# Performance work log

Hardware: AMD Instinct MI355X
Metric: run time of the kernel (lower is better)

## Reference

```python
import jax, jax.numpy as jnp
import numpy as np

N = 50000      # nodes per graph
E = 600000     # edges per graph
IN_DIM = 512
HID = 128
LAYERS = 2


def setup_inputs() -> dict:
    key = jax.random.key(0)
    ks = jax.random.split(key, 24)
    s = 0.05
    inp = {
        "src_fea": jax.random.normal(ks[0], (N, IN_DIM), jnp.float32),
        "trg_fea": jax.random.normal(ks[1], (N, IN_DIM), jnp.float32),
        "src_row": jax.random.randint(ks[2], (E,), 0, N, jnp.int32),
        "src_col": jax.random.randint(ks[3], (E,), 0, N, jnp.int32),
        "trg_row": jax.random.randint(ks[4], (E,), 0, N, jnp.int32),
        "trg_col": jax.random.randint(ks[5], (E,), 0, N, jnp.int32),
        # fx: Linear(in,hid)+GELU+Linear(hid,hid)+GELU
        "fxW1": jax.random.normal(ks[6], (IN_DIM, HID), jnp.float32) * s,
        "fxb1": jnp.zeros((HID,), jnp.float32),
        "fxW2": jax.random.normal(ks[7], (HID, HID), jnp.float32) * s,
        "fxb2": jnp.zeros((HID,), jnp.float32),
        # edge_att_mlp: Linear(2h,20)+ReLU+Linear(20,10)+ReLU+Linear(10,1)+ReLU
        "eaW1": jax.random.normal(ks[8], (2 * HID, 20), jnp.float32) * s,
        "eab1": jnp.zeros((20,), jnp.float32),
        "eaW2": jax.random.normal(ks[9], (20, 10), jnp.float32) * s,
        "eab2": jnp.zeros((10,), jnp.float32),
        "eaW3": jax.random.normal(ks[10], (10, 1), jnp.float32) * s,
        "eab3": jnp.zeros((1,), jnp.float32),
        # GraphConv (PyG-style, bias=False): out = x@Wroot + agg@Wrel
        "convWroot": jax.random.normal(ks[11], (LAYERS, HID, HID), jnp.float32) * s,
        "convWrel": jax.random.normal(ks[12], (LAYERS, HID, HID), jnp.float32) * s,
    }
    return inp


def _fx(x, W1, b1, W2, b2):
    h = jax.nn.gelu(x @ W1 + b1, approximate=False)
    return jax.nn.gelu(h @ W2 + b2, approximate=False)


def _edge_att(e, eaW1, eab1, eaW2, eab2, eaW3, eab3):
    h = jax.nn.relu(e @ eaW1 + eab1)
    h = jax.nn.relu(h @ eaW2 + eab2)
    h = jax.nn.relu(h @ eaW3 + eab3)
    return jax.nn.sigmoid(h)  # [E,1]


def _graph_conv(x, row, col, ew, Wroot, Wrel):
    # message from source (row) gathered, weighted, aggregated at target (col)
    msg = ew[:, None] * x[row]                                  # [E,h]
    agg = jax.ops.segment_sum(msg, col, num_segments=N)         # [N,h]
    return x @ Wroot + agg @ Wrel


def _branch(x0, row, col, convWroot, convWrel, eaW1, eab1, eaW2, eab2, eaW3, eab3, hard):
    xs, cfds = [], []
    x = x0
    for i in range(LAYERS):
        edge_rep = jnp.concatenate([x[row], x[col]], axis=-1)    # [E,2h]
        att = _edge_att(edge_rep, eaW1, eab1, eaW2, eab2, eaW3, eab3)[:, 0]
        wc = (att + hard) * 0.5
        wo = 1.0 - wc
        x = jax.nn.soft_sign(_graph_conv(x, row, col, wc, convWroot[i], convWrel[i]))
        cfd = jax.nn.soft_sign(_graph_conv(x, row, col, wo, convWroot[i], convWrel[i]))
        xs.append(x)
        cfds.append(cfd)
    return xs, cfds


def reference(src_fea, trg_fea, src_row, src_col, trg_row, trg_col,
              fxW1, fxb1, fxW2, fxb2,
              eaW1, eab1, eaW2, eab2, eaW3, eab3,
              convWroot, convWrel):
    src1 = _fx(src_fea, fxW1, fxb1, fxW2, fxb2)
    trg1 = _fx(trg_fea, fxW1, fxb1, fxW2, fxb2)
    ea = (eaW1, eab1, eaW2, eab2, eaW3, eab3)
    xs_s, cf_s = _branch(src1, src_row, src_col, convWroot, convWrel, *ea, 0.0)
    xs_t, cf_t = _branch(trg1, trg_row, trg_col, convWroot, convWrel, *ea, 0.0)
    # stack: [src1, xs_s..., trg1, xs_t..., cf_s..., cf_t...] -> [2+2*LAYERS+2*LAYERS? no: 10, N, h]
    return jnp.stack([src1] + xs_s + [trg1] + xs_t + cf_s + cf_t, axis=0)
```

## Files before the change

kernel.cpp:

```cpp
#include <hip/hip_runtime.h>
#include <math.h>
#include <stdint.h>


typedef __attribute__((ext_vector_type(8))) short bh8;
typedef __attribute__((ext_vector_type(4))) float f4;

__device__ __forceinline__ float relu_f(float x) { return x > 0.f ? x : 0.f; }

__device__ __forceinline__ unsigned short f2bf(float f) {
    union { float f; unsigned u; } v; v.f = f;
    unsigned r = v.u + 0x7FFF + ((v.u >> 16) & 1);
    return (unsigned short)(r >> 16);
}
__device__ __forceinline__ float bf2f(unsigned short b) {
    union { unsigned u; float f; } v; v.u = ((unsigned)b) << 16;
    return v.f;
}

template<int ACT>
__device__ __forceinline__ float act_fn(float x) {
    if (ACT == 1) return 0.5f * x * (1.f + erff(x * 0.70710678118654752f));
    if (ACT == 2) return x / (1.f + fabsf(x));
    return x;
}

__device__ __forceinline__ void emit_p_phase(short* As, short* Bs,
                                             const short* __restrict__ W56,
                                             short* __restrict__ P,
                                             int row0, int M, int t)
{
    #pragma unroll
    for (int p = 0; p < 4; ++p) {
        int idx = t + 256 * p;
        int r = idx >> 4;
        int c = (idx & 15) * 8;
        *(bh8*)&Bs[r * 136 + c] = *(const bh8*)(W56 + r * 128 + c);
    }
    __syncthreads();
    const int lane = t & 63, w = t >> 6, l15 = lane & 15, l4 = lane >> 4;
    f4 accP[4];
    #pragma unroll
    for (int ni = 0; ni < 4; ++ni) accP[ni] = (f4){0.f, 0.f, 0.f, 0.f};
    #pragma unroll
    for (int kk = 0; kk < 4; ++kk) {
        bh8 a = *(const bh8*)&As[(w * 16 + l15) * 136 + kk * 32 + l4 * 8];
        #pragma unroll
        for (int ni = 0; ni < 4; ++ni) {
            bh8 b = *(const bh8*)&Bs[(ni * 16 + l15) * 136 + kk * 32 + l4 * 8];
            accP[ni] = __builtin_amdgcn_mfma_f32_16x16x32_bf16(a, b, accP[ni], 0, 0, 0);
        }
    }
    #pragma unroll
    for (int ni = 0; ni < 4; ++ni) {
        int col = ni * 16 + l15;
        #pragma unroll
        for (int r = 0; r < 4; ++r) {
            int row = row0 + w * 16 + l4 * 4 + r;
            if (row < M) P[(size_t)row * 64 + col] = (short)f2bf(accP[ni][r]);
        }
    }
}

template<int K, int AF, int ACT, bool BIAS, bool WF32, bool WB16, bool EMITP>
__global__ __launch_bounds__(256, 2)
void mfma_gemm(const void* __restrict__ X0a, const void* __restrict__ X0b,
               const short* __restrict__ W0t, const float* __restrict__ bias,
               float* __restrict__ outfA, short* __restrict__ outbA,
               float* __restrict__ outfB, short* __restrict__ outbB,
               const short* __restrict__ W56,
               short* __restrict__ PA, short* __restrict__ PB, int M)
{
    constexpr int BK  = 64;
    constexpr int LDA = EMITP ? 136 : 72;
    __shared__ short As[64 * LDA];
    __shared__ short Bs[128 * 72];

    const int half = gridDim.x >> 1;
    int bid = blockIdx.x;
    const int g1 = bid >= half;
    bid -= g1 ? half : 0;
    const void* X0v = g1 ? X0b : X0a;
    float* outf = g1 ? outfB : outfA;
    short* outb = g1 ? outbB : outbA;
    short* P    = g1 ? PB : PA;

    const int t    = threadIdx.x;
    const int row0 = bid * 64;
    const int lane = t & 63;
    const int w    = t >> 6;
    const int wr   = w & 1;
    const int wc   = w >> 1;
    const int l15  = lane & 15;
    const int l4   = lane >> 4;

    f4 acc[2][4];
    #pragma unroll
    for (int i = 0; i < 2; ++i)
        #pragma unroll
        for (int j = 0; j < 4; ++j)
            acc[i][j] = (f4){0.f, 0.f, 0.f, 0.f};

    const int ar = t >> 3;
    const int ac = (t & 7) * 8;

    #pragma unroll 1
    for (int k0 = 0; k0 < K; k0 += BK) {
        __syncthreads();
        #pragma unroll
        for (int p = 0; p < 2; ++p) {
            int r    = ar + p * 32;
            int grow = row0 + r;
            bh8 sv = {0, 0, 0, 0, 0, 0, 0, 0};
            if (AF == 0) {
                if (grow < M) {
                    const float* src = (const float*)X0v + (size_t)grow * K + k0 + ac;
                    float4 v0 = *(const float4*)src;
                    float4 v1 = *(const float4*)(src + 4);
                    sv[0] = (short)f2bf(v0.x); sv[1] = (short)f2bf(v0.y);
                    sv[2] = (short)f2bf(v0.z); sv[3] = (short)f2bf(v0.w);
                    sv[4] = (short)f2bf(v1.x); sv[5] = (short)f2bf(v1.y);
                    sv[6] = (short)f2bf(v1.z); sv[7] = (short)f2bf(v1.w);
                }
            } else {
                if (grow < M)
                    sv = *(const bh8*)((const short*)X0v + (size_t)grow * K + k0 + ac);
            }
            *(bh8*)&As[r * LDA + ac] = sv;
        }
        #pragma unroll
        for (int p = 0; p < 4; ++p) {
            int r = ar + p * 32;
            *(bh8*)&Bs[r * 72 + ac] = *(const bh8*)(W0t + (size_t)r * K + k0 + ac);
        }
        __syncthreads();
        #pragma unroll
        for (int kk = 0; kk < 2; ++kk) {
            bh8 a[2], b[4];
            #pragma unroll
            for (int mi = 0; mi < 2; ++mi)
                a[mi] = *(const bh8*)&As[(wr*32 + mi*16 + l15) * LDA + kk*32 + l4*8];
            #pragma unroll
            for (int ni = 0; ni < 4; ++ni)
                b[ni] = *(const bh8*)&Bs[(wc*64 + ni*16 + l15) * 72 + kk*32 + l4*8];
            #pragma unroll
            for (int mi = 0; mi < 2; ++mi)
                #pragma unroll
                for (int ni = 0; ni < 4; ++ni)
                    acc[mi][ni] = __builtin_amdgcn_mfma_f32_16x16x32_bf16(
                        a[mi], b[ni], acc[mi][ni], 0, 0, 0);
        }
    }

    if (EMITP) __syncthreads();
    #pragma unroll
    for (int mi = 0; mi < 2; ++mi) {
        #pragma unroll
        for (int ni = 0; ni < 4; ++ni) {
            int col = wc * 64 + ni * 16 + l15;
            float bv = BIAS ? bias[col] : 0.f;
            #pragma unroll
            for (int r = 0; r < 4; ++r) {
                int rloc = wr * 32 + mi * 16 + l4 * 4 + r;
                int row  = row0 + rloc;
                float v = act_fn<ACT>(acc[mi][ni][r] + bv);
                unsigned short bb = f2bf(v);
                if (row < M) {
                    if (WF32) outf[(size_t)row * 128 + col] = v;
                    if (WB16) outb[(size_t)row * 128 + col] = (short)bb;
                }
                if (EMITP) As[rloc * LDA + col] = (short)bb;
            }
        }
    }
    if (EMITP) emit_p_phase(As, Bs, W56, P, row0, M, t);
}

template<int MODE, bool WB16, bool EMITP>
__global__ __launch_bounds__(256, 2)
void conv_fused(const short* __restrict__ XbA, const short* __restrict__ XbB,
                const int* __restrict__ coffA, const int* __restrict__ coffB,
                const int* __restrict__ crowA, const int* __restrict__ crowB,
                const float* __restrict__ attcA, const float* __restrict__ attcB,
                const short* __restrict__ Wroot, const short* __restrict__ Wrel,
                const short* __restrict__ W56,
                float* __restrict__ outfA, float* __restrict__ outfB,
                short* __restrict__ outbA, short* __restrict__ outbB,
                short* __restrict__ PA, short* __restrict__ PB, int M)
{
    constexpr int LDA = 136;
    __shared__ short As[64 * LDA];
    __shared__ short Bs[128 * 72];

    const int half = gridDim.x >> 1;
    int bid = blockIdx.x;
    const int g1 = bid >= half;
    bid -= g1 ? half : 0;
    const short* Xb   = g1 ? XbB   : XbA;
    const int*   coff = g1 ? coffB : coffA;
    const int*   crow = g1 ? crowB : crowA;
    const float* attc = g1 ? attcB : attcA;
    float* outf = g1 ? outfB : outfA;
    short* outb = g1 ? outbB : outbA;
    short* P    = g1 ? PB : PA;

    const int t    = threadIdx.x;
    const int row0 = bid * 64;
    const int lane = t & 63;
    const int w    = t >> 6;
    const int wr   = w & 1;
    const int wc   = w >> 1;
    const int l15  = lane & 15;
    const int l4   = lane >> 4;

    {
        const int g  = t >> 4;
        const int li = t & 15;
        #pragma unroll 1
        for (int q = 0; q < 4; ++q) {
            int rloc = g * 4 + q;
            int n = row0 + rloc;
            float a8[8] = {0.f, 0.f, 0.f, 0.f, 0.f, 0.f, 0.f, 0.f};
            if (n < M) {
                int p  = coff[n];
                int pe = coff[n + 1];
                for (; p + 3 < pe; p += 4) {
                    float w0 = attc[p],     w1 = attc[p + 1];
                    float w2 = attc[p + 2], w3 = attc[p + 3];
                    int r0 = crow[p],     r1 = crow[p + 1];
                    int r2 = crow[p + 2], r3 = crow[p + 3];
                    w0 = MODE ? fmaf(-0.5f, w0, 1.f) : 0.5f * w0;
                    w1 = MODE ? fmaf(-0.5f, w1, 1.f) : 0.5f * w1;
                    w2 = MODE ? fmaf(-0.5f, w2, 1.f) : 0.5f * w2;
                    w3 = MODE ? fmaf(-0.5f, w3, 1.f) : 0.5f * w3;
                    bh8 v0 = *(const bh8*)&Xb[(size_t)r0 * 128 + li * 8];
                    bh8 v1 = *(const bh8*)&Xb[(size_t)r1 * 128 + li * 8];
                    bh8 v2 = *(const bh8*)&Xb[(size_t)r2 * 128 + li * 8];
                    bh8 v3 = *(const bh8*)&Xb[(size_t)r3 * 128 + li * 8];
                    #pragma unroll
                    for (int j = 0; j < 8; ++j) {
                        a8[j] = fmaf(w0, bf2f((unsigned short)v0[j]), a8[j]);
                        a8[j] = fmaf(w1, bf2f((unsigned short)v1[j]), a8[j]);
                        a8[j] = fmaf(w2, bf2f((unsigned short)v2[j]), a8[j]);
                        a8[j] = fmaf(w3, bf2f((unsigned short)v3[j]), a8[j]);
                    }
                }
                for (; p < pe; ++p) {
                    float w0 = attc[p];
                    int   r0 = crow[p];
                    w0 = MODE ? fmaf(-0.5f, w0, 1.f) : 0.5f * w0;
                    bh8 v0 = *(const bh8*)&Xb[(size_t)r0 * 128 + li * 8];
                    #pragma unroll
                    for (int j = 0; j < 8; ++j)
                        a8[j] = fmaf(w0, bf2f((unsigned short)v0[j]), a8[j]);
                }
            }
            bh8 o;
            #pragma unroll
            for (int j = 0; j < 8; ++j) o[j] = (short)f2bf(a8[j]);
            *(bh8*)&As[rloc * LDA + li * 8] = o;
        }
    }
    __syncthreads();

    f4 acc[2][4];
    #pragma unroll
    for (int i = 0; i < 2; ++i)
        #pragma unroll
        for (int j = 0; j < 4; ++j)
            acc[i][j] = (f4){0.f, 0.f, 0.f, 0.f};

    const int ar = t >> 3;
    const int ac = (t & 7) * 8;

    #pragma unroll 1
    for (int k0 = 0; k0 < 128; k0 += 64) {
        if (k0) __syncthreads();
        #pragma unroll
        for (int p = 0; p < 4; ++p) {
            int r = ar + p * 32;
            *(bh8*)&Bs[r * 72 + ac] = *(const bh8*)(Wrel + (size_t)r * 128 + k0 + ac);
        }
        __syncthreads();
        #pragma unroll
        for (int kk = 0; kk < 2; ++kk) {
            bh8 a[2], b[4];
            #pragma unroll
            for (int mi = 0; mi < 2; ++mi)
                a[mi] = *(const bh8*)&As[(wr*32 + mi*16 + l15) * LDA + k0 + kk*32 + l4*8];
            #pragma unroll
            for (int ni = 0; ni < 4; ++ni)
                b[ni] = *(const bh8*)&Bs[(wc*64 + ni*16 + l15) * 72 + kk*32 + l4*8];
            #pragma unroll
            for (int mi = 0; mi < 2; ++mi)
                #pragma unroll
                for (int ni = 0; ni < 4; ++ni)
                    acc[mi][ni] = __builtin_amdgcn_mfma_f32_16x16x32_bf16(
                        a[mi], b[ni], acc[mi][ni], 0, 0, 0);
        }
    }

    #pragma unroll 1
    for (int k0 = 0; k0 < 128; k0 += 64) {
        __syncthreads();
        #pragma unroll
        for (int p = 0; p < 2; ++p) {
            int r    = ar + p * 32;
            int grow = row0 + r;
            bh8 sv = {0, 0, 0, 0, 0, 0, 0, 0};
            if (grow < M)
                sv = *(const bh8*)(Xb + (size_t)grow * 128 + k0 + ac);
            *(bh8*)&As[r * LDA + ac] = sv;
        }
        #pragma unroll
        for (int p = 0; p < 4; ++p) {
            int r = ar + p * 32;
            *(bh8*)&Bs[r * 72 + ac] = *(const bh8*)(Wroot + (size_t)r * 128 + k0 + ac);
        }
        __syncthreads();
        #pragma unroll
        for (int kk = 0; kk < 2; ++kk) {
            bh8 a[2], b[4];
            #pragma unroll
            for (int mi = 0; mi < 2; ++mi)
                a[mi] = *(const bh8*)&As[(wr*32 + mi*16 + l15) * LDA + kk*32 + l4*8];
            #pragma unroll
            for (int ni = 0; ni < 4; ++ni)
                b[ni] = *(const bh8*)&Bs[(wc*64 + ni*16 + l15) * 72 + kk*32 + l4*8];
            #pragma unroll
            for (int mi = 0; mi < 2; ++mi)
                #pragma unroll
                for (int ni = 0; ni < 4; ++ni)
                    acc[mi][ni] = __builtin_amdgcn_mfma_f32_16x16x32_bf16(
                        a[mi], b[ni], acc[mi][ni], 0, 0, 0);
        }
    }

    if (EMITP) __syncthreads();
    #pragma unroll
    for (int mi = 0; mi < 2; ++mi) {
        #pragma unroll
        for (int ni = 0; ni < 4; ++ni) {
            int col = wc * 64 + ni * 16 + l15;
            #pragma unroll
            for (int r = 0; r < 4; ++r) {
                int rloc = wr * 32 + mi * 16 + l4 * 4 + r;
                int row  = row0 + rloc;
                float v = act_fn<2>(acc[mi][ni][r]);
                unsigned short bb = f2bf(v);
                if (row < M) {
                    outf[(size_t)row * 128 + col] = v;
                    if (WB16) outb[(size_t)row * 128 + col] = (short)bb;
                }
                if (EMITP) As[rloc * LDA + col] = (short)bb;
            }
        }
    }
    if (EMITP) emit_p_phase(As, Bs, W56, P, row0, M, t);
}

__global__ void prep_all(const float* __restrict__ eaW1, const float* __restrict__ fxW1,
                         const float* __restrict__ fxW2, const float* __restrict__ convWroot,
                         const float* __restrict__ convWrel,
                         short* __restrict__ w56, short* __restrict__ fxW1t,
                         short* __restrict__ fxW2t, short* __restrict__ wrt,
                         short* __restrict__ wlt)
{
    int i = blockIdx.x * 256 + threadIdx.x;
    if (i < 64 * 128) {
        int j = i >> 7, k = i & 127;
        float v = 0.f;
        if (j < 20)                  v = eaW1[k * 20 + j];
        else if (j >= 32 && j < 52)  v = eaW1[(128 + k) * 20 + (j - 32)];
        w56[i] = (short)f2bf(v);
        return;
    }
    i -= 64 * 128;
    if (i < 512 * 128) {
        int k = i >> 7, n = i & 127;
        fxW1t[(size_t)n * 512 + k] = (short)f2bf(fxW1[i]);
        return;
    }
    i -= 512 * 128;
    if (i < 128 * 128) {
        int k = i >> 7, n = i & 127;
        fxW2t[n * 128 + k] = (short)f2bf(fxW2[i]);
        return;
    }
    i -= 128 * 128;
    if (i < 2 * 128 * 128) {
        int L = i >> 14, r = i & 16383;
        int k = r >> 7, n = r & 127;
        wrt[L * 16384 + n * 128 + k] = (short)f2bf(convWroot[i]);
        return;
    }
    i -= 2 * 128 * 128;
    if (i < 2 * 128 * 128) {
        int L = i >> 14, r = i & 16383;
        int k = r >> 7, n = r & 127;
        wlt[L * 16384 + n * 128 + k] = (short)f2bf(convWrel[i]);
    }
}

__global__ __launch_bounds__(256)
void edge_att_both(const short* __restrict__ PS, const short* __restrict__ PT,
                   const int* __restrict__ rowS, const int* __restrict__ colS,
                   const int* __restrict__ rowT, const int* __restrict__ colT,
                   const int* __restrict__ eposS, const int* __restrict__ eposT,
                   const float* __restrict__ eab1, const float* __restrict__ eaW2,
                   const float* __restrict__ eab2, const float* __restrict__ eaW3,
                   const float* __restrict__ eab3,
                   float* __restrict__ attcS, float* __restrict__ attcT, int E)
{
    __shared__ float w2[200], b2s[10], w3s[10], sb1[20], sb3;
    int t = threadIdx.x;
    if (t < 200) w2[t] = eaW2[t];
    if (t < 20)  sb1[t] = eab1[t];
    if (t < 10)  { b2s[t] = eab2[t]; w3s[t] = eaW3[t]; }
    if (t == 0)  sb3 = eab3[0];
    __syncthreads();

    int idx = blockIdx.x * 256 + t;
    if (idx >= 2 * E) return;
    const int g1 = idx >= E;
    const int e  = idx - (g1 ? E : 0);
    const short* P    = g1 ? PT : PS;
    const int*   row  = g1 ? rowT : rowS;
    const int*   col  = g1 ? colT : colS;
    const int*   epos = g1 ? eposT : eposS;
    float*       attc = g1 ? attcT : attcS;

    int r = row[e], c = col[e];
    const unsigned short* p1 = (const unsigned short*)P + (size_t)r * 64;
    const unsigned short* p2 = (const unsigned short*)P + (size_t)c * 64 + 32;

    bh8 a0 = *(const bh8*)&p1[0];
    bh8 a1 = *(const bh8*)&p1[8];
    ushort4 a2 = *(const ushort4*)&p1[16];
    bh8 b0 = *(const bh8*)&p2[0];
    bh8 b1 = *(const bh8*)&p2[8];
    ushort4 b2 = *(const ushort4*)&p2[16];

    float h1[20];
    #pragma unroll
    for (int j = 0; j < 8; ++j)
        h1[j] = relu_f(bf2f((unsigned short)a0[j]) + bf2f((unsigned short)b0[j]) + sb1[j]);
    #pragma unroll
    for (int j = 0; j < 8; ++j)
        h1[8 + j] = relu_f(bf2f((unsigned short)a1[j]) + bf2f((unsigned short)b1[j]) + sb1[8 + j]);
    h1[16] = relu_f(bf2f(a2.x) + bf2f(b2.x) + sb1[16]);
    h1[17] = relu_f(bf2f(a2.y) + bf2f(b2.y) + sb1[17]);
    h1[18] = relu_f(bf2f(a2.z) + bf2f(b2.z) + sb1[18]);
    h1[19] = relu_f(bf2f(a2.w) + bf2f(b2.w) + sb1[19]);

    float h3 = sb3;
    #pragma unroll
    for (int j2 = 0; j2 < 10; ++j2) {
        float s = b2s[j2];
        #pragma unroll
        for (int j = 0; j < 20; ++j)
            s = fmaf(h1[j], w2[j * 10 + j2], s);
        h3 = fmaf(relu_f(s), w3s[j2], h3);
    }
    h3 = relu_f(h3);
    attc[epos[e]] = 1.f / (1.f + expf(-h3));
}

__global__ void hist_both(const int* __restrict__ colS, const int* __restrict__ colT,
                          int* __restrict__ deg, int N, int E)
{
    int idx = blockIdx.x * 256 + threadIdx.x;
    if (idx >= 2 * E) return;
    const int g1 = idx >= E;
    const int e  = idx - (g1 ? E : 0);
    int c = (g1 ? colT : colS)[e];
    atomicAdd(&deg[(size_t)g1 * N + c], 1);
}

__device__ __forceinline__ int block_incl_scan(int v, int* wsum)
{
    int lane = threadIdx.x & 63;
    int w    = threadIdx.x >> 6;
    #pragma unroll
    for (int off = 1; off < 64; off <<= 1) {
        int t = __shfl_up(v, off);
        if (lane >= off) v += t;
    }
    if (lane == 63) wsum[w] = v;
    __syncthreads();
    int add = 0;
    for (int j = 0; j < w; ++j) add += wsum[j];
    return v + add;
}

__global__ __launch_bounds__(256)
void scanA_both(const int* __restrict__ deg, int* __restrict__ coffS,
                int* __restrict__ coffT, int* __restrict__ bsum, int N)
{
    __shared__ int wsum[4];
    int gy = blockIdx.y;
    const int* d = deg + (size_t)gy * N;
    int* coff    = gy ? coffT : coffS;
    int* bs      = bsum + gy * 256;
    int i = blockIdx.x * 256 + threadIdx.x;
    int orig = (i < N) ? d[i] : 0;
    int v = block_incl_scan(orig, wsum);
    if (i < N) coff[i] = v - orig;
    if (threadIdx.x == 255) bs[blockIdx.x] = v;
}

__global__ __launch_bounds__(256)
void scanB_both(const int* __restrict__ bsum, int* __restrict__ boff, int nb)
{
    __shared__ int wsum[4];
    int gy = blockIdx.y;
    const int* bs = bsum + gy * 256;
    int* bo       = boff + gy * 256;
    int tid = threadIdx.x;
    int orig = (tid < nb) ? bs[tid] : 0;
    int v = block_incl_scan(orig, wsum);
    if (tid < nb) bo[tid] = v - orig;
}

__global__ __launch_bounds__(256)
void scanC_both(int* __restrict__ coffS, int* __restrict__ coffT,
                const int* __restrict__ boff, int* __restrict__ curS,
                int* __restrict__ curT, int N, int E)
{
    int gy = blockIdx.y;
    int* coff = gy ? coffT : coffS;
    int* cur  = gy ? curT  : curS;
    const int* bo = boff + gy * 256;
    int i = blockIdx.x * 256 + threadIdx.x;
    if (i < N) {
        int v = coff[i] + bo[i >> 8];
        coff[i] = v;
        cur[i]  = v;
    }
    if (i == 0) coff[N] = E;
}

__global__ __launch_bounds__(256)
void fill_both(const int* __restrict__ rowS, const int* __restrict__ colS,
               const int* __restrict__ rowT, const int* __restrict__ colT,
               int* __restrict__ curS, int* __restrict__ curT,
               int* __restrict__ crowS, int* __restrict__ crowT,
               int* __restrict__ eposS, int* __restrict__ eposT, int E)
{
    int idx = blockIdx.x * 256 + threadIdx.x;
    if (idx >= 2 * E) return;
    const int g1 = idx >= E;
    const int e  = idx - (g1 ? E : 0);
    const int* row = g1 ? rowT : rowS;
    const int* col = g1 ? colT : colS;
    int* cur  = g1 ? curT  : curS;
    int* crow = g1 ? crowT : crowS;
    int* epos = g1 ? eposT : eposS;
    int c = col[e];
    int p = atomicAdd(&cur[c], 1);
    crow[p] = row[e];
    epos[e] = p;
}


extern "C" void kernel_launch(void* const* d_in, const int* in_sizes, int n_in,
                              void* d_out, int out_size, void* d_ws, size_t ws_size,
                              hipStream_t stream)
{
    const float* src_fea = (const float*)d_in[0];
    const float* trg_fea = (const float*)d_in[1];
    const int*   src_row = (const int*)d_in[2];
    const int*   src_col = (const int*)d_in[3];
    const int*   trg_row = (const int*)d_in[4];
    const int*   trg_col = (const int*)d_in[5];
    const float* fxW1 = (const float*)d_in[6];
    const float* fxb1 = (const float*)d_in[7];
    const float* fxW2 = (const float*)d_in[8];
    const float* fxb2 = (const float*)d_in[9];
    const float* eaW1 = (const float*)d_in[10];
    const float* eab1 = (const float*)d_in[11];
    const float* eaW2 = (const float*)d_in[12];
    const float* eab2 = (const float*)d_in[13];
    const float* eaW3 = (const float*)d_in[14];
    const float* eab3 = (const float*)d_in[15];
    const float* convWroot = (const float*)d_in[16];
    const float* convWrel  = (const float*)d_in[17];

    const int N = in_sizes[0] / 512;
    const int E = in_sizes[2];

    float* out = (float*)d_out;
    const size_t slot_sz = (size_t)N * 128;
    auto slot = [&](int i) { return out + (size_t)i * slot_sz; };

    float* fp    = (float*)d_ws;
    float* attcS = fp; fp += E;
    float* attcT = fp; fp += E;
    int* ip    = (int*)fp;
    int* deg   = ip; ip += 2 * N;
    int* bsum  = ip; ip += 512;
    int* boff  = ip; ip += 512;
    int* coffS = ip; ip += N + 2;
    int* coffT = ip; ip += N + 2;
    int* curS  = ip; ip += N;
    int* curT  = ip; ip += N;
    int* crowS = ip; ip += E;
    int* crowT = ip; ip += E;
    int* eposS = ip; ip += E;
    int* eposT = ip; ip += E;
    short* sp = (short*)((((uintptr_t)ip) + 255) & ~(uintptr_t)255);
    short* xb0   = sp; sp += slot_sz;
    short* xb1   = sp; sp += slot_sz;
    short* xsbS[2]; short* xsbT[2];
    xsbS[0] = sp; sp += slot_sz;
    xsbS[1] = sp; sp += slot_sz;
    xsbT[0] = sp; sp += slot_sz;
    xsbT[1] = sp; sp += slot_sz;
    short* PS    = sp; sp += (size_t)N * 64;
    short* PT    = sp; sp += (size_t)N * 64;
    short* w56   = sp; sp += 64 * 128;
    short* fxW1t = sp; sp += 128 * 512;
    short* fxW2t = sp; sp += 128 * 128;
    short* wrt   = sp; sp += 2 * 128 * 128;
    short* wlt   = sp; sp += 2 * 128 * 128;

    const int prep_total = 64*128 + 512*128 + 128*128 + 2*128*128 + 2*128*128;
    prep_all<<<(prep_total + 255) / 256, 256, 0, stream>>>(
        eaW1, fxW1, fxW2, convWroot, convWrel, w56, fxW1t, fxW2t, wrt, wlt);

    const int gb = (N + 63) / 64;
    short* hS = xsbS[0];
    short* hT = xsbT[0];
    mfma_gemm<512, 0, 1, true, false, true, false><<<2 * gb, 256, 0, stream>>>(
        src_fea, trg_fea, fxW1t, fxb1,
        nullptr, hS, nullptr, hT, nullptr, nullptr, nullptr, N);
    mfma_gemm<128, 1, 1, true, true, true, true><<<2 * gb, 256, 0, stream>>>(
        hS, hT, fxW2t, fxb2,
        slot(0), xb0, slot(3), xb1, w56, PS, PT, N);

    const int e2grid  = (2 * E + 255) / 256;
    const int nchunks = (N + 255) / 256;
    hipMemsetAsync(deg, 0, (size_t)2 * N * sizeof(int), stream);
    hist_both<<<e2grid, 256, 0, stream>>>(src_col, trg_col, deg, N, E);
    scanA_both<<<dim3(nchunks, 2), 256, 0, stream>>>(deg, coffS, coffT, bsum, N);
    scanB_both<<<dim3(1, 2), 256, 0, stream>>>(bsum, boff, nchunks);
    scanC_both<<<dim3(nchunks, 2), 256, 0, stream>>>(coffS, coffT, boff, curS, curT, N, E);
    fill_both<<<e2grid, 256, 0, stream>>>(src_row, src_col, trg_row, trg_col,
                                          curS, curT, crowS, crowT, eposS, eposT, E);

    short* xbS = xb0;
    short* xbT = xb1;
    for (int L = 0; L < 2; ++L) {
        float* xs_s = slot(1 + L);
        float* xs_t = slot(4 + L);
        float* cf_s = slot(6 + L);
        float* cf_t = slot(8 + L);
        const short* WrT = wrt + (size_t)L * 16384;
        const short* WlT = wlt + (size_t)L * 16384;

        edge_att_both<<<e2grid, 256, 0, stream>>>(PS, PT, src_row, src_col,
            trg_row, trg_col, eposS, eposT, eab1, eaW2, eab2, eaW3, eab3,
            attcS, attcT, E);

        if (L == 0)
            conv_fused<0, true, true><<<2 * gb, 256, 0, stream>>>(
                xbS, xbT, coffS, coffT, crowS, crowT, attcS, attcT,
                WrT, WlT, w56, xs_s, xs_t, xsbS[L], xsbT[L], PS, PT, N);
        else
            conv_fused<0, true, false><<<2 * gb, 256, 0, stream>>>(
                xbS, xbT, coffS, coffT, crowS, crowT, attcS, attcT,
                WrT, WlT, nullptr, xs_s, xs_t, xsbS[L], xsbT[L], nullptr, nullptr, N);

        conv_fused<1, false, false><<<2 * gb, 256, 0, stream>>>(
            xsbS[L], xsbT[L], coffS, coffT, crowS, crowT, attcS, attcT,
            WrT, WlT, nullptr, cf_s, cf_t, nullptr, nullptr, nullptr, nullptr, N);

        xbS = xsbS[L];
        xbT = xsbT[L];
    }
}
```

Measured before the change: 652.7 us.

## Interleave four rows' gathers in aggregation, fuse histogram into prep, iterate edges in CSR order

The aggregation loop in conv_fused now walks four destination rows together, two edges per row per step, so more independent gather loads are in flight per thread instead of finishing one row before starting the next. The degree histogram is merged into the weight-prep kernel as extra blocks, which saves a launch. edge_att_both now runs in CSR order using new sorted row/col arrays, so the attention write is contiguous and the scattered epos indirection is gone. The cost is more register pressure from four accumulator sets, plus divergence when rows have uneven degrees.

```diff
diff --git a/kernel.cpp b/kernel.cpp
--- a/kernel.cpp
+++ b/kernel.cpp
@@ -216,49 +216,62 @@
     {
         const int g  = t >> 4;
         const int li = t & 15;
-        #pragma unroll 1
+        const int n0 = row0 + g * 4;
+        int p[4], pe[4];
+        #pragma unroll
         for (int q = 0; q < 4; ++q) {
-            int rloc = g * 4 + q;
-            int n = row0 + rloc;
-            float a8[8] = {0.f, 0.f, 0.f, 0.f, 0.f, 0.f, 0.f, 0.f};
-            if (n < M) {
-                int p  = coff[n];
-                int pe = coff[n + 1];
-                for (; p + 3 < pe; p += 4) {
-                    float w0 = attc[p],     w1 = attc[p + 1];
-                    float w2 = attc[p + 2], w3 = attc[p + 3];
-                    int r0 = crow[p],     r1 = crow[p + 1];
-                    int r2 = crow[p + 2], r3 = crow[p + 3];
-                    w0 = MODE ? fmaf(-0.5f, w0, 1.f) : 0.5f * w0;
-                    w1 = MODE ? fmaf(-0.5f, w1, 1.f) : 0.5f * w1;
-                    w2 = MODE ? fmaf(-0.5f, w2, 1.f) : 0.5f * w2;
-                    w3 = MODE ? fmaf(-0.5f, w3, 1.f) : 0.5f * w3;
-                    bh8 v0 = *(const bh8*)&Xb[(size_t)r0 * 128 + li * 8];
-                    bh8 v1 = *(const bh8*)&Xb[(size_t)r1 * 128 + li * 8];
-                    bh8 v2 = *(const bh8*)&Xb[(size_t)r2 * 128 + li * 8];
-                    bh8 v3 = *(const bh8*)&Xb[(size_t)r3 * 128 + li * 8];
-                    #pragma unroll
-                    for (int j = 0; j < 8; ++j) {
-                        a8[j] = fmaf(w0, bf2f((unsigned short)v0[j]), a8[j]);
-                        a8[j] = fmaf(w1, bf2f((unsigned short)v1[j]), a8[j]);
-                        a8[j] = fmaf(w2, bf2f((unsigned short)v2[j]), a8[j]);
-                        a8[j] = fmaf(w3, bf2f((unsigned short)v3[j]), a8[j]);
-                    }
+            int n = n0 + q;
+            bool ok = n < M;
+            p[q]  = ok ? coff[n]     : 0;
+            pe[q] = ok ? coff[n + 1] : 0;
+        }
+        float a8[4][8];
+        #pragma unroll
+        for (int q = 0; q < 4; ++q)
+            #pragma unroll
+            for (int j = 0; j < 8; ++j) a8[q][j] = 0.f;
+
+        bool more = (p[0] < pe[0]) || (p[1] < pe[1]) ||
+                    (p[2] < pe[2]) || (p[3] < pe[3]);
+        while (more) {
+            float w0[4], w1[4];
+            bh8 v0[4], v1[4];
+            #pragma unroll
+            for (int q = 0; q < 4; ++q) {
+                if (p[q] < pe[q]) {
+                    w0[q] = attc[p[q]];
+                    v0[q] = *(const bh8*)&Xb[(size_t)crow[p[q]] * 128 + li * 8];
                 }
-                for (; p < pe; ++p) {
-                    float w0 = attc[p];
-                    int   r0 = crow[p];
-                    w0 = MODE ? fmaf(-0.5f, w0, 1.f) : 0.5f * w0;
-                    bh8 v0 = *(const bh8*)&Xb[(size_t)r0 * 128 + li * 8];
+                if (p[q] + 1 < pe[q]) {
+                    w1[q] = attc[p[q] + 1];
+                    v1[q] = *(const bh8*)&Xb[(size_t)crow[p[q] + 1] * 128 + li * 8];
+                }
+            }
+            more = false;
+            #pragma unroll
+            for (int q = 0; q < 4; ++q) {
+                if (p[q] < pe[q]) {
+                    float wv = MODE ? fmaf(-0.5f, w0[q], 1.f) : 0.5f * w0[q];
                     #pragma unroll
                     for (int j = 0; j < 8; ++j)
-                        a8[j] = fmaf(w0, bf2f((unsigned short)v0[j]), a8[j]);
+                        a8[q][j] = fmaf(wv, bf2f((unsigned short)v0[q][j]), a8[q][j]);
                 }
+                if (p[q] + 1 < pe[q]) {
+                    float wv = MODE ? fmaf(-0.5f, w1[q], 1.f) : 0.5f * w1[q];
+                    #pragma unroll
+                    for (int j = 0; j < 8; ++j)
+                        a8[q][j] = fmaf(wv, bf2f((unsigned short)v1[q][j]), a8[q][j]);
+                }
+                p[q] += 2;
+                more = more || (p[q] < pe[q]);
             }
+        }
+        #pragma unroll
+        for (int q = 0; q < 4; ++q) {
             bh8 o;
             #pragma unroll
-            for (int j = 0; j < 8; ++j) o[j] = (short)f2bf(a8[j]);
-            *(bh8*)&As[rloc * LDA + li * 8] = o;
+            for (int j = 0; j < 8; ++j) o[j] = (short)f2bf(a8[q][j]);
+            *(bh8*)&As[(g * 4 + q) * LDA + li * 8] = o;
         }
     }
     __syncthreads();
@@ -359,13 +372,24 @@
     if (EMITP) emit_p_phase(As, Bs, W56, P, row0, M, t);
 }
 
-__global__ void prep_all(const float* __restrict__ eaW1, const float* __restrict__ fxW1,
-                         const float* __restrict__ fxW2, const float* __restrict__ convWroot,
-                         const float* __restrict__ convWrel,
-                         short* __restrict__ w56, short* __restrict__ fxW1t,
-                         short* __restrict__ fxW2t, short* __restrict__ wrt,
-                         short* __restrict__ wlt)
-{
+__global__ void prep_hist(const float* __restrict__ eaW1, const float* __restrict__ fxW1,
+                          const float* __restrict__ fxW2, const float* __restrict__ convWroot,
+                          const float* __restrict__ convWrel,
+                          short* __restrict__ w56, short* __restrict__ fxW1t,
+                          short* __restrict__ fxW2t, short* __restrict__ wrt,
+                          short* __restrict__ wlt,
+                          const int* __restrict__ colS, const int* __restrict__ colT,
+                          int* __restrict__ deg, int N, int E, int prepBlocks)
+{
+    if ((int)blockIdx.x >= prepBlocks) {
+        int idx = (blockIdx.x - prepBlocks) * 256 + threadIdx.x;
+        if (idx >= 2 * E) return;
+        const int g1 = idx >= E;
+        const int e  = idx - (g1 ? E : 0);
+        int c = (g1 ? colT : colS)[e];
+        atomicAdd(&deg[(size_t)g1 * N + c], 1);
+        return;
+    }
     int i = blockIdx.x * 256 + threadIdx.x;
     if (i < 64 * 128) {
         int j = i >> 7, k = i & 127;
@@ -404,9 +428,8 @@
 
 __global__ __launch_bounds__(256)
 void edge_att_both(const short* __restrict__ PS, const short* __restrict__ PT,
-                   const int* __restrict__ rowS, const int* __restrict__ colS,
-                   const int* __restrict__ rowT, const int* __restrict__ colT,
-                   const int* __restrict__ eposS, const int* __restrict__ eposT,
+                   const int* __restrict__ crowS, const int* __restrict__ ccolS,
+                   const int* __restrict__ crowT, const int* __restrict__ ccolT,
                    const float* __restrict__ eab1, const float* __restrict__ eaW2,
                    const float* __restrict__ eab2, const float* __restrict__ eaW3,
                    const float* __restrict__ eab3,
@@ -423,14 +446,13 @@
     int idx = blockIdx.x * 256 + t;
     if (idx >= 2 * E) return;
     const int g1 = idx >= E;
-    const int e  = idx - (g1 ? E : 0);
+    const int p  = idx - (g1 ? E : 0);
     const short* P    = g1 ? PT : PS;
-    const int*   row  = g1 ? rowT : rowS;
-    const int*   col  = g1 ? colT : colS;
-    const int*   epos = g1 ? eposT : eposS;
+    const int*   crow = g1 ? crowT : crowS;
+    const int*   ccol = g1 ? ccolT : ccolS;
     float*       attc = g1 ? attcT : attcS;
 
-    int r = row[e], c = col[e];
+    int r = crow[p], c = ccol[p];
     const unsigned short* p1 = (const unsigned short*)P + (size_t)r * 64;
     const unsigned short* p2 = (const unsigned short*)P + (size_t)c * 64 + 32;
 
@@ -463,18 +485,7 @@
         h3 = fmaf(relu_f(s), w3s[j2], h3);
     }
     h3 = relu_f(h3);
-    attc[epos[e]] = 1.f / (1.f + expf(-h3));
-}
-
-__global__ void hist_both(const int* __restrict__ colS, const int* __restrict__ colT,
-                          int* __restrict__ deg, int N, int E)
-{
-    int idx = blockIdx.x * 256 + threadIdx.x;
-    if (idx >= 2 * E) return;
-    const int g1 = idx >= E;
-    const int e  = idx - (g1 ? E : 0);
-    int c = (g1 ? colT : colS)[e];
-    atomicAdd(&deg[(size_t)g1 * N + c], 1);
+    attc[p] = 1.f / (1.f + expf(-h3));
 }
 
 __device__ __forceinline__ int block_incl_scan(int v, int* wsum)
@@ -545,7 +556,7 @@
                const int* __restrict__ rowT, const int* __restrict__ colT,
                int* __restrict__ curS, int* __restrict__ curT,
                int* __restrict__ crowS, int* __restrict__ crowT,
-               int* __restrict__ eposS, int* __restrict__ eposT, int E)
+               int* __restrict__ ccolS, int* __restrict__ ccolT, int E)
 {
     int idx = blockIdx.x * 256 + threadIdx.x;
     if (idx >= 2 * E) return;
@@ -555,11 +566,11 @@
     const int* col = g1 ? colT : colS;
     int* cur  = g1 ? curT  : curS;
     int* crow = g1 ? crowT : crowS;
-    int* epos = g1 ? eposT : eposS;
+    int* ccol = g1 ? ccolT : ccolS;
     int c = col[e];
     int p = atomicAdd(&cur[c], 1);
     crow[p] = row[e];
-    epos[e] = p;
+    ccol[p] = c;
 }
 
 
@@ -606,8 +617,8 @@
     int* curT  = ip; ip += N;
     int* crowS = ip; ip += E;
     int* crowT = ip; ip += E;
-    int* eposS = ip; ip += E;
-    int* eposT = ip; ip += E;
+    int* ccolS = ip; ip += E;
+    int* ccolT = ip; ip += E;
     short* sp = (short*)((((uintptr_t)ip) + 255) & ~(uintptr_t)255);
     short* xb0   = sp; sp += slot_sz;
     short* xb1   = sp; sp += slot_sz;
@@ -624,9 +635,15 @@
     short* wrt   = sp; sp += 2 * 128 * 128;
     short* wlt   = sp; sp += 2 * 128 * 128;
 
-    const int prep_total = 64*128 + 512*128 + 128*128 + 2*128*128 + 2*128*128;
-    prep_all<<<(prep_total + 255) / 256, 256, 0, stream>>>(
-        eaW1, fxW1, fxW2, convWroot, convWrel, w56, fxW1t, fxW2t, wrt, wlt);
+    const int e2grid  = (2 * E + 255) / 256;
+    const int nchunks = (N + 255) / 256;
+
+    hipMemsetAsync(deg, 0, (size_t)2 * N * sizeof(int), stream);
+    const int prep_total  = 64*128 + 512*128 + 128*128 + 2*128*128 + 2*128*128;
+    const int prepBlocks  = (prep_total + 255) / 256;
+    prep_hist<<<prepBlocks + e2grid, 256, 0, stream>>>(
+        eaW1, fxW1, fxW2, convWroot, convWrel, w56, fxW1t, fxW2t, wrt, wlt,
+        src_col, trg_col, deg, N, E, prepBlocks);
 
     const int gb = (N + 63) / 64;
     short* hS = xsbS[0];
@@ -638,15 +655,11 @@
         hS, hT, fxW2t, fxb2,
         slot(0), xb0, slot(3), xb1, w56, PS, PT, N);
 
-    const int e2grid  = (2 * E + 255) / 256;
-    const int nchunks = (N + 255) / 256;
-    hipMemsetAsync(deg, 0, (size_t)2 * N * sizeof(int), stream);
-    hist_both<<<e2grid, 256, 0, stream>>>(src_col, trg_col, deg, N, E);
     scanA_both<<<dim3(nchunks, 2), 256, 0, stream>>>(deg, coffS, coffT, bsum, N);
     scanB_both<<<dim3(1, 2), 256, 0, stream>>>(bsum, boff, nchunks);
     scanC_both<<<dim3(nchunks, 2), 256, 0, stream>>>(coffS, coffT, boff, curS, curT, N, E);
     fill_both<<<e2grid, 256, 0, stream>>>(src_row, src_col, trg_row, trg_col,
-                                          curS, curT, crowS, crowT, eposS, eposT, E);
+                                          curS, curT, crowS, crowT, ccolS, ccolT, E);
 
     short* xbS = xb0;
     short* xbT = xb1;
@@ -658,9 +671,8 @@
         const short* WrT = wrt + (size_t)L * 16384;
         const short* WlT = wlt + (size_t)L * 16384;
 
-        edge_att_both<<<e2grid, 256, 0, stream>>>(PS, PT, src_row, src_col,
-            trg_row, trg_col, eposS, eposT, eab1, eaW2, eab2, eaW3, eab3,
-            attcS, attcT, E);
+        edge_att_both<<<e2grid, 256, 0, stream>>>(PS, PT, crowS, ccolS,
+            crowT, ccolT, eab1, eaW2, eab2, eaW3, eab3, attcS, attcT, E);
 
         if (L == 0)
             conv_fused<0, true, true><<<2 * gb, 256, 0, stream>>>(
```

After: 737.8 us. +13.0%, slower.

## Fuse edge-attention MLP into conv kernel and merge histogram with weight prep

Applied to the files above, without the earlier changes.

Edge-attention scores are now computed inside the first conv kernel for each layer, over the CSR edge range owned by the block. Target-side projections are staged in shared memory, and attc is written in CSR order, which removes the separate edge_att kernel and the epos scatter indirection. The degree histogram is also folded into the weight-prep launch to save a kernel launch. In exchange, P buffers are double-buffered so the fused kernel does not read and write the same P, and the conv kernel gains extra shared memory and a serial attention phase before aggregation that may reduce occupancy.

```diff
diff --git a/kernel.cpp b/kernel.cpp
--- a/kernel.cpp
+++ b/kernel.cpp
@@ -176,21 +176,28 @@
     if (EMITP) emit_p_phase(As, Bs, W56, P, row0, M, t);
 }
 
-template<int MODE, bool WB16, bool EMITP>
+template<int MODE, bool WB16, bool EMITP, bool ATTGEN>
 __global__ __launch_bounds__(256, 2)
 void conv_fused(const short* __restrict__ XbA, const short* __restrict__ XbB,
                 const int* __restrict__ coffA, const int* __restrict__ coffB,
                 const int* __restrict__ crowA, const int* __restrict__ crowB,
-                const float* __restrict__ attcA, const float* __restrict__ attcB,
+                const int* __restrict__ ccolA, const int* __restrict__ ccolB,
+                float* attcA, float* attcB,
+                const short* __restrict__ PinA, const short* __restrict__ PinB,
+                const float* __restrict__ eab1, const float* __restrict__ eaW2,
+                const float* __restrict__ eab2, const float* __restrict__ eaW3,
+                const float* __restrict__ eab3,
                 const short* __restrict__ Wroot, const short* __restrict__ Wrel,
                 const short* __restrict__ W56,
                 float* __restrict__ outfA, float* __restrict__ outfB,
                 short* __restrict__ outbA, short* __restrict__ outbB,
-                short* __restrict__ PA, short* __restrict__ PB, int M)
+                short* __restrict__ PoutA, short* __restrict__ PoutB, int M)
 {
     constexpr int LDA = 136;
     __shared__ short As[64 * LDA];
     __shared__ short Bs[128 * 72];
+    __shared__ float ea[ATTGEN ? 241 : 1];
+    __shared__ __align__(16) short p2t[ATTGEN ? 64 * 24 : 8];
 
     const int half = gridDim.x >> 1;
     int bid = blockIdx.x;
@@ -199,10 +206,12 @@
     const short* Xb   = g1 ? XbB   : XbA;
     const int*   coff = g1 ? coffB : coffA;
     const int*   crow = g1 ? crowB : crowA;
-    const float* attc = g1 ? attcB : attcA;
+    const int*   ccol = g1 ? ccolB : ccolA;
+    float*       attc = g1 ? attcB : attcA;
+    const short* Pin  = g1 ? PinB  : PinA;
     float* outf = g1 ? outfB : outfA;
     short* outb = g1 ? outbB : outbA;
-    short* P    = g1 ? PB : PA;
+    short* Pout = g1 ? PoutB : PoutA;
 
     const int t    = threadIdx.x;
     const int row0 = bid * 64;
@@ -212,6 +221,68 @@
     const int wc   = w >> 1;
     const int l15  = lane & 15;
     const int l4   = lane >> 4;
+
+    if (ATTGEN) {
+        if (t < 200)       ea[t] = eaW2[t];
+        else if (t < 210)  ea[t] = eab2[t - 200];
+        else if (t < 220)  ea[t] = eaW3[t - 210];
+        else if (t < 240)  ea[t] = eab1[t - 220];
+        else if (t == 240) ea[240] = eab3[0];
+        if (t < 64) {
+            int row = row0 + t;
+            if (row < M) {
+                const unsigned short* src = (const unsigned short*)Pin + (size_t)row * 64 + 32;
+                *(bh8*)&p2t[t * 24]          = *(const bh8*)&src[0];
+                *(bh8*)&p2t[t * 24 + 8]      = *(const bh8*)&src[8];
+                *(ushort4*)&p2t[t * 24 + 16] = *(const ushort4*)&src[16];
+            }
+        }
+        __syncthreads();
+        int rend = row0 + 64; if (rend > M) rend = M;
+        const int pb  = coff[row0];
+        const int peb = coff[rend];
+        const float* w2v = ea;
+        const float* b2v = ea + 200;
+        const float* w3v = ea + 210;
+        const float* b1v = ea + 220;
+        const float  b3v = ea[240];
+        for (int p = pb + t; p < peb; p += 256) {
+            int r = crow[p], c = ccol[p];
+            const unsigned short* p1 = (const unsigned short*)Pin + (size_t)r * 64;
+            bh8 a0 = *(const bh8*)&p1[0];
+            bh8 a1 = *(const bh8*)&p1[8];
+            ushort4 a2 = *(const ushort4*)&p1[16];
+            const short* q2 = &p2t[(c - row0) * 24];
+            bh8 c0 = *(const bh8*)&q2[0];
+            bh8 c1 = *(const bh8*)&q2[8];
+            ushort4 c2 = *(const ushort4*)&q2[16];
+
+            float h1[20];
+            #pragma unroll
+            for (int j = 0; j < 8; ++j)
+                h1[j] = relu_f(bf2f((unsigned short)a0[j]) + bf2f((unsigned short)c0[j]) + b1v[j]);
+            #pragma unroll
+            for (int j = 0; j < 8; ++j)
+                h1[8 + j] = relu_f(bf2f((unsigned short)a1[j]) + bf2f((unsigned short)c1[j]) + b1v[8 + j]);
+            h1[16] = relu_f(bf2f(a2.x) + bf2f(c2.x) + b1v[16]);
+            h1[17] = relu_f(bf2f(a2.y) + bf2f(c2.y) + b1v[17]);
+            h1[18] = relu_f(bf2f(a2.z) + bf2f(c2.z) + b1v[18]);
+            h1[19] = relu_f(bf2f(a2.w) + bf2f(c2.w) + b1v[19]);
+
+            float h3 = b3v;
+            #pragma unroll
+            for (int j2 = 0; j2 < 10; ++j2) {
+                float s = b2v[j2];
+                #pragma unroll
+                for (int j = 0; j < 20; ++j)
+                    s = fmaf(h1[j], w2v[j * 10 + j2], s);
+                h3 = fmaf(relu_f(s), w3v[j2], h3);
+            }
+            h3 = relu_f(h3);
+            attc[p] = 1.f / (1.f + expf(-h3));
+        }
+        __syncthreads();
+    }
 
     {
         const int g  = t >> 4;
@@ -356,16 +427,27 @@
             }
         }
     }
-    if (EMITP) emit_p_phase(As, Bs, W56, P, row0, M, t);
-}
-
-__global__ void prep_all(const float* __restrict__ eaW1, const float* __restrict__ fxW1,
-                         const float* __restrict__ fxW2, const float* __restrict__ convWroot,
-                         const float* __restrict__ convWrel,
-                         short* __restrict__ w56, short* __restrict__ fxW1t,
-                         short* __restrict__ fxW2t, short* __restrict__ wrt,
-                         short* __restrict__ wlt)
-{
+    if (EMITP) emit_p_phase(As, Bs, W56, Pout, row0, M, t);
+}
+
+__global__ void prep_hist(const float* __restrict__ eaW1, const float* __restrict__ fxW1,
+                          const float* __restrict__ fxW2, const float* __restrict__ convWroot,
+                          const float* __restrict__ convWrel,
+                          short* __restrict__ w56, short* __restrict__ fxW1t,
+                          short* __restrict__ fxW2t, short* __restrict__ wrt,
+                          short* __restrict__ wlt,
+                          const int* __restrict__ colS, const int* __restrict__ colT,
+                          int* __restrict__ deg, int N, int E, int prepBlocks)
+{
+    if ((int)blockIdx.x >= prepBlocks) {
+        int idx = (blockIdx.x - prepBlocks) * 256 + threadIdx.x;
+        if (idx >= 2 * E) return;
+        const int g1 = idx >= E;
+        const int e  = idx - (g1 ? E : 0);
+        int c = (g1 ? colT : colS)[e];
+        atomicAdd(&deg[(size_t)g1 * N + c], 1);
+        return;
+    }
     int i = blockIdx.x * 256 + threadIdx.x;
     if (i < 64 * 128) {
         int j = i >> 7, k = i & 127;
@@ -400,81 +482,6 @@
         int k = r >> 7, n = r & 127;
         wlt[L * 16384 + n * 128 + k] = (short)f2bf(convWrel[i]);
     }
-}
-
-__global__ __launch_bounds__(256)
-void edge_att_both(const short* __restrict__ PS, const short* __restrict__ PT,
-                   const int* __restrict__ rowS, const int* __restrict__ colS,
-                   const int* __restrict__ rowT, const int* __restrict__ colT,
-                   const int* __restrict__ eposS, const int* __restrict__ eposT,
-                   const float* __restrict__ eab1, const float* __restrict__ eaW2,
-                   const float* __restrict__ eab2, const float* __restrict__ eaW3,
-                   const float* __restrict__ eab3,
-                   float* __restrict__ attcS, float* __restrict__ attcT, int E)
-{
-    __shared__ float w2[200], b2s[10], w3s[10], sb1[20], sb3;
-    int t = threadIdx.x;
-    if (t < 200) w2[t] = eaW2[t];
-    if (t < 20)  sb1[t] = eab1[t];
-    if (t < 10)  { b2s[t] = eab2[t]; w3s[t] = eaW3[t]; }
-    if (t == 0)  sb3 = eab3[0];
-    __syncthreads();
-
-    int idx = blockIdx.x * 256 + t;
-    if (idx >= 2 * E) return;
-    const int g1 = idx >= E;
-    const int e  = idx - (g1 ? E : 0);
-    const short* P    = g1 ? PT : PS;
-    const int*   row  = g1 ? rowT : rowS;
-    const int*   col  = g1 ? colT : colS;
-    const int*   epos = g1 ? eposT : eposS;
-    float*       attc = g1 ? attcT : attcS;
-
-    int r = row[e], c = col[e];
-    const unsigned short* p1 = (const unsigned short*)P + (size_t)r * 64;
-    const unsigned short* p2 = (const unsigned short*)P + (size_t)c * 64 + 32;
-
-    bh8 a0 = *(const bh8*)&p1[0];
-    bh8 a1 = *(const bh8*)&p1[8];
-    ushort4 a2 = *(const ushort4*)&p1[16];
-    bh8 b0 = *(const bh8*)&p2[0];
-    bh8 b1 = *(const bh8*)&p2[8];
-    ushort4 b2 = *(const ushort4*)&p2[16];
-
-    float h1[20];
-    #pragma unroll
-    for (int j = 0; j < 8; ++j)
-        h1[j] = relu_f(bf2f((unsigned short)a0[j]) + bf2f((unsigned short)b0[j]) + sb1[j]);
-    #pragma unroll
-    for (int j = 0; j < 8; ++j)
-        h1[8 + j] = relu_f(bf2f((unsigned short)a1[j]) + bf2f((unsigned short)b1[j]) + sb1[8 + j]);
-    h1[16] = relu_f(bf2f(a2.x) + bf2f(b2.x) + sb1[16]);
-    h1[17] = relu_f(bf2f(a2.y) + bf2f(b2.y) + sb1[17]);
-    h1[18] = relu_f(bf2f(a2.z) + bf2f(b2.z) + sb1[18]);
-    h1[19] = relu_f(bf2f(a2.w) + bf2f(b2.w) + sb1[19]);
-
-    float h3 = sb3;
-    #pragma unroll
-    for (int j2 = 0; j2 < 10; ++j2) {
-        float s = b2s[j2];
-        #pragma unroll
-        for (int j = 0; j < 20; ++j)
-            s = fmaf(h1[j], w2[j * 10 + j2], s);
-        h3 = fmaf(relu_f(s), w3s[j2], h3);
-    }
-    h3 = relu_f(h3);
-    attc[epos[e]] = 1.f / (1.f + expf(-h3));
-}
-
-__global__ void hist_both(const int* __restrict__ colS, const int* __restrict__ colT,
-                          int* __restrict__ deg, int N, int E)
-{
-    int idx = blockIdx.x * 256 + threadIdx.x;
-    if (idx >= 2 * E) return;
-    const int g1 = idx >= E;
-    const int e  = idx - (g1 ? E : 0);
-    int c = (g1 ? colT : colS)[e];
-    atomicAdd(&deg[(size_t)g1 * N + c], 1);
 }
 
 __device__ __forceinline__ int block_incl_scan(int v, int* wsum)
@@ -545,7 +552,7 @@
                const int* __restrict__ rowT, const int* __restrict__ colT,
                int* __restrict__ curS, int* __restrict__ curT,
                int* __restrict__ crowS, int* __restrict__ crowT,
-               int* __restrict__ eposS, int* __restrict__ eposT, int E)
+               int* __restrict__ ccolS, int* __restrict__ ccolT, int E)
 {
     int idx = blockIdx.x * 256 + threadIdx.x;
     if (idx >= 2 * E) return;
@@ -555,11 +562,11 @@
     const int* col = g1 ? colT : colS;
     int* cur  = g1 ? curT  : curS;
     int* crow = g1 ? crowT : crowS;
-    int* epos = g1 ? eposT : eposS;
+    int* ccol = g1 ? ccolT : ccolS;
     int c = col[e];
     int p = atomicAdd(&cur[c], 1);
     crow[p] = row[e];
-    epos[e] = p;
+    ccol[p] = c;
 }
 
 
@@ -606,8 +613,8 @@
     int* curT  = ip; ip += N;
     int* crowS = ip; ip += E;
     int* crowT = ip; ip += E;
-    int* eposS = ip; ip += E;
-    int* eposT = ip; ip += E;
+    int* ccolS = ip; ip += E;
+    int* ccolT = ip; ip += E;
     short* sp = (short*)((((uintptr_t)ip) + 255) & ~(uintptr_t)255);
     short* xb0   = sp; sp += slot_sz;
     short* xb1   = sp; sp += slot_sz;
@@ -616,17 +623,25 @@
     xsbS[1] = sp; sp += slot_sz;
     xsbT[0] = sp; sp += slot_sz;
     xsbT[1] = sp; sp += slot_sz;
-    short* PS    = sp; sp += (size_t)N * 64;
-    short* PT    = sp; sp += (size_t)N * 64;
+    short* PS0   = sp; sp += (size_t)N * 64;
+    short* PT0   = sp; sp += (size_t)N * 64;
+    short* PS1   = sp; sp += (size_t)N * 64;
+    short* PT1   = sp; sp += (size_t)N * 64;
     short* w56   = sp; sp += 64 * 128;
     short* fxW1t = sp; sp += 128 * 512;
     short* fxW2t = sp; sp += 128 * 128;
     short* wrt   = sp; sp += 2 * 128 * 128;
     short* wlt   = sp; sp += 2 * 128 * 128;
 
-    const int prep_total = 64*128 + 512*128 + 128*128 + 2*128*128 + 2*128*128;
-    prep_all<<<(prep_total + 255) / 256, 256, 0, stream>>>(
-        eaW1, fxW1, fxW2, convWroot, convWrel, w56, fxW1t, fxW2t, wrt, wlt);
+    const int e2grid  = (2 * E + 255) / 256;
+    const int nchunks = (N + 255) / 256;
+
+    hipMemsetAsync(deg, 0, (size_t)2 * N * sizeof(int), stream);
+    const int prep_total  = 64*128 + 512*128 + 128*128 + 2*128*128 + 2*128*128;
+    const int prepBlocks  = (prep_total + 255) / 256;
+    prep_hist<<<prepBlocks + e2grid, 256, 0, stream>>>(
+        eaW1, fxW1, fxW2, convWroot, convWrel, w56, fxW1t, fxW2t, wrt, wlt,
+        src_col, trg_col, deg, N, E, prepBlocks);
 
     const int gb = (N + 63) / 64;
     short* hS = xsbS[0];
@@ -636,17 +651,13 @@
         nullptr, hS, nullptr, hT, nullptr, nullptr, nullptr, N);
     mfma_gemm<128, 1, 1, true, true, true, true><<<2 * gb, 256, 0, stream>>>(
         hS, hT, fxW2t, fxb2,
-        slot(0), xb0, slot(3), xb1, w56, PS, PT, N);
-
-    const int e2grid  = (2 * E + 255) / 256;
-    const int nchunks = (N + 255) / 256;
-    hipMemsetAsync(deg, 0, (size_t)2 * N * sizeof(int), stream);
-    hist_both<<<e2grid, 256, 0, stream>>>(src_col, trg_col, deg, N, E);
+        slot(0), xb0, slot(3), xb1, w56, PS0, PT0, N);
+
     scanA_both<<<dim3(nchunks, 2), 256, 0, stream>>>(deg, coffS, coffT, bsum, N);
     scanB_both<<<dim3(1, 2), 256, 0, stream>>>(bsum, boff, nchunks);
     scanC_both<<<dim3(nchunks, 2), 256, 0, stream>>>(coffS, coffT, boff, curS, curT, N, E);
     fill_both<<<e2grid, 256, 0, stream>>>(src_row, src_col, trg_row, trg_col,
-                                          curS, curT, crowS, crowT, eposS, eposT, E);
+                                          curS, curT, crowS, crowT, ccolS, ccolT, E);
 
     short* xbS = xb0;
     short* xbT = xb1;
@@ -657,22 +668,23 @@
         float* cf_t = slot(8 + L);
         const short* WrT = wrt + (size_t)L * 16384;
         const short* WlT = wlt + (size_t)L * 16384;
-
-        edge_att_both<<<e2grid, 256, 0, stream>>>(PS, PT, src_row, src_col,
-            trg_row, trg_col, eposS, eposT, eab1, eaW2, eab2, eaW3, eab3,
-            attcS, attcT, E);
+        const short* PinS = L ? PS1 : PS0;
+        const short* PinT = L ? PT1 : PT0;
 
         if (L == 0)
-            conv_fused<0, true, true><<<2 * gb, 256, 0, stream>>>(
-                xbS, xbT, coffS, coffT, crowS, crowT, attcS, attcT,
-                WrT, WlT, w56, xs_s, xs_t, xsbS[L], xsbT[L], PS, PT, N);
+            conv_fused<0, true, true, true><<<2 * gb, 256, 0, stream>>>(
+                xbS, xbT, coffS, coffT, crowS, crowT, ccolS, ccolT,
+                attcS, attcT, PinS, PinT, eab1, eaW2, eab2, eaW3, eab3,
+                WrT, WlT, w56, xs_s, xs_t, xsbS[L], xsbT[L], PS1, PT1, N);
         else
-            conv_fused<0, true, false><<<2 * gb, 256, 0, stream>>>(
-                xbS, xbT, coffS, coffT, crowS, crowT, attcS, attcT,
+            conv_fused<0, true, false, true><<<2 * gb, 256, 0, stream>>>(
+                xbS, xbT, coffS, coffT, crowS, crowT, ccolS, ccolT,
+                attcS, attcT, PinS, PinT, eab1, eaW2, eab2, eaW3, eab3,
                 WrT, WlT, nullptr, xs_s, xs_t, xsbS[L], xsbT[L], nullptr, nullptr, N);
 
-        conv_fused<1, false, false><<<2 * gb, 256, 0, stream>>>(
-            xsbS[L], xsbT[L], coffS, coffT, crowS, crowT, attcS, attcT,
+        conv_fused<1, false, false, false><<<2 * gb, 256, 0, stream>>>(
+            xsbS[L], xsbT[L], coffS, coffT, crowS, crowT, ccolS, ccolT,
+            attcS, attcT, nullptr, nullptr, eab1, eaW2, eab2, eaW3, eab3,
             WrT, WlT, nullptr, cf_s, cf_t, nullptr, nullptr, nullptr, nullptr, N);
 
         xbS = xsbS[L];
```

Result: slower. 816.0 us (+25.0%).
